# Kernel tuning notes

Measured on AMD Instinct MI355X. Metric: run time of the kernel, lower is better.

The kernel has to match this reference:

```python
import jax, jax.numpy as jnp
import numpy as np

D_MODEL = 1024
N_HEADS = 16


def setup_inputs() -> dict:
    key = jax.random.key(0)
    ks = jax.random.split(key, 5)
    B, T, C = 4, 2048, D_MODEL
    x = jax.random.normal(ks[0], (B, T, C), dtype=jnp.float32)
    s = 1.0 / np.sqrt(C)
    W_attn = jax.random.normal(ks[1], (C, 3 * C), dtype=jnp.float32) * s
    b_attn = jnp.zeros((3 * C,), dtype=jnp.float32)
    W_proj = jax.random.normal(ks[2], (C, C), dtype=jnp.float32) * s
    b_proj = jnp.zeros((C,), dtype=jnp.float32)
    return {"x": x, "W_attn": W_attn, "b_attn": b_attn, "W_proj": W_proj, "b_proj": b_proj}


def reference(x, W_attn, b_attn, W_proj, b_proj):
    B, T, C = x.shape
    H = N_HEADS
    hd = C // H
    qkv = x @ W_attn + b_attn                      # [B,T,3C]
    q, k, v = jnp.split(qkv, 3, axis=-1)
    # reshape to [B,H,T,hd]
    q = q.reshape(B, T, H, hd).transpose(0, 2, 1, 3)
    k = k.reshape(B, T, H, hd).transpose(0, 2, 1, 3)
    v = v.reshape(B, T, H, hd).transpose(0, 2, 1, 3)
    scale = 1.0 / jnp.sqrt(jnp.asarray(hd, dtype=x.dtype))
    aff = jnp.einsum('bhqd,bhkd->bhqk', q, k) * scale   # [B,H,T,T]
    causal = jnp.tril(jnp.ones((T, T), dtype=bool))
    aff = jnp.where(causal, aff, jnp.asarray(-jnp.inf, dtype=aff.dtype))
    p = jax.nn.softmax(aff, axis=-1)
    y = jnp.einsum('bhqk,bhkd->bhqd', p, v)             # [B,H,T,hd]
    y = y.transpose(0, 2, 1, 3).reshape(B, T, C)
    return y @ W_proj + b_proj
```

## Files before the change

kernel.cpp:

```cpp
#include <hip/hip_runtime.h>
#include <stdint.h>
#include <math.h>

typedef __attribute__((ext_vector_type(8))) __bf16 bf16x8;
typedef __attribute__((ext_vector_type(4))) __bf16 bf16x4;
typedef __attribute__((ext_vector_type(4))) float f32x4;
typedef __attribute__((ext_vector_type(16))) float f32x16;

#define MFMA16(A, B, C) __builtin_amdgcn_mfma_f32_16x16x32_bf16((A), (B), (C), 0, 0, 0)
#define MFMA32(A, B, C) __builtin_amdgcn_mfma_f32_32x32x16_bf16((A), (B), (C), 0, 0, 0)

#if defined(__has_builtin)
#if __has_builtin(__builtin_amdgcn_exp2f)
#define EXP2(x) __builtin_amdgcn_exp2f(x)
#else
#define EXP2(x) exp2f(x)
#endif
#else
#define EXP2(x) exp2f(x)
#endif

static constexpr int kT  = 2048;
static constexpr int kC  = 1024;
static constexpr int kHD = 64;
#define QSCALE 0.1803368801111204f

__device__ __forceinline__ void g2l16(const void* g, void* l) {
  __builtin_amdgcn_global_load_lds(
      (const __attribute__((address_space(1))) uint32_t*)g,
      (__attribute__((address_space(3))) uint32_t*)l, 16, 0, 0);
}

__global__ __launch_bounds__(256) void k_convert_x(const float* __restrict__ x,
                                                   __bf16* __restrict__ xb) {
  int i = (blockIdx.x * 256 + threadIdx.x) * 4;
  f32x4 v = *(const f32x4*)(x + i);
  bf16x4 o;
  o[0] = (__bf16)v[0]; o[1] = (__bf16)v[1]; o[2] = (__bf16)v[2]; o[3] = (__bf16)v[3];
  *(bf16x4*)(xb + i) = o;
}

__global__ __launch_bounds__(256) void k_transpose_w(const float* __restrict__ src,
                                                     __bf16* __restrict__ dst, int N) {
  __shared__ float t[32][33];
  int k0 = blockIdx.x * 32, n0 = blockIdx.y * 32;
  int c = threadIdx.x & 31, r = threadIdx.x >> 5;
#pragma unroll
  for (int i = 0; i < 4; ++i)
    t[r + i * 8][c] = src[(size_t)(k0 + r + i * 8) * N + n0 + c];
  __syncthreads();
#pragma unroll
  for (int i = 0; i < 4; ++i)
    dst[(size_t)(n0 + r + i * 8) * 1024 + k0 + c] = (__bf16)t[c][r + i * 8];
}

static constexpr int GK = 1024;
static constexpr int GNT = GK / 32;

template <int MODE>
__global__ __launch_bounds__(256, 3) void k_gemm(const __bf16* __restrict__ A,
                                                 const __bf16* __restrict__ Bw,
                                                 const float* __restrict__ bias,
                                                 __bf16* __restrict__ qo,
                                                 __bf16* __restrict__ ko,
                                                 __bf16* __restrict__ vo,
                                                 float* __restrict__ out) {
  __shared__ __bf16 As[3][128 * 32];
  __shared__ __bf16 Bs[3][128 * 32];

  const int tid = threadIdx.x;
  const int wave = tid >> 6, lane = tid & 63;
  const int lo = lane & 15, hi = lane >> 4;
  const int wr = wave & 1, wc = wave >> 1;

  constexpr int NBN = (MODE == 0) ? 24 : 8;
  const int nwg = (int)gridDim.x;
  const int id = (int)blockIdx.x;
  const int wg = (id & 7) * (nwg >> 3) + (id >> 3);
  const int bm = wg / NBN, bn = wg % NBN;
  const int m0 = bm * 128, n0 = bn * 128;

  const int rG0 = tid >> 2, gG0 = (tid & 3) ^ ((rG0 >> 1) & 3);
  const int rG1 = (tid + 256) >> 2, gG1 = ((tid + 256) & 3) ^ ((rG1 >> 1) & 3);
  const __bf16* gaA0 = A + (size_t)(m0 + rG0) * GK + gG0 * 8;
  const __bf16* gaA1 = A + (size_t)(m0 + rG1) * GK + gG1 * 8;
  const __bf16* gbB0 = Bw + (size_t)(n0 + rG0) * GK + gG0 * 8;
  const __bf16* gbB1 = Bw + (size_t)(n0 + rG1) * GK + gG1 * 8;

  const int fsw = (hi ^ ((lo >> 1) & 3)) * 8;
  const int offA = (wr * 64 + lo) * 32 + fsw;
  const int offB = (wc * 64 + lo) * 32 + fsw;

  f32x4 acc[4][4] = {};

#define GSTAGE(jt, bufi)                                  \
  {                                                       \
    g2l16(gaA0 + (jt) * 32, &As[(bufi)][tid * 8]);        \
    g2l16(gaA1 + (jt) * 32, &As[(bufi)][2048 + tid * 8]); \
    g2l16(gbB0 + (jt) * 32, &Bs[(bufi)][tid * 8]);        \
    g2l16(gbB1 + (jt) * 32, &Bs[(bufi)][2048 + tid * 8]); \
  }

  GSTAGE(0, 0);
  GSTAGE(1, 1);
  asm volatile("s_waitcnt vmcnt(4)" ::: "memory");
  __builtin_amdgcn_s_barrier();
  __builtin_amdgcn_sched_barrier(0);

  int rb = 0, rs = 2;
  for (int j = 0; j < GNT; ++j) {
    const __bf16* Ab = &As[rb][0];
    const __bf16* Bb = &Bs[rb][0];
    if (j < GNT - 2) GSTAGE(j + 2, rs);
    bf16x8 af[4], bfr[4];
#pragma unroll
    for (int m = 0; m < 4; ++m) af[m] = *(const bf16x8*)&Ab[offA + m * 512];
#pragma unroll
    for (int n = 0; n < 4; ++n) bfr[n] = *(const bf16x8*)&Bb[offB + n * 512];
    __builtin_amdgcn_s_setprio(1);
#pragma unroll
    for (int m = 0; m < 4; ++m)
#pragma unroll
      for (int n = 0; n < 4; ++n)
        acc[m][n] = MFMA16(af[m], bfr[n], acc[m][n]);
    __builtin_amdgcn_s_setprio(0);
    if (j < GNT - 2) {
      asm volatile("s_waitcnt vmcnt(4)" ::: "memory");
    } else if (j == GNT - 2) {
      asm volatile("s_waitcnt vmcnt(0)" ::: "memory");
    }
    if (j < GNT - 1) {
      __builtin_amdgcn_s_barrier();
      __builtin_amdgcn_sched_barrier(0);
    }
    rb = (rb == 2) ? 0 : rb + 1;
    rs = (rs == 2) ? 0 : rs + 1;
  }
#undef GSTAGE

  if (MODE == 0) {
#pragma unroll
    for (int nj = 0; nj < 4; ++nj) {
      int gn = n0 + wc * 64 + nj * 16 + lo;
      float bv = bias[gn];
      int which = gn >> 10;
      int c = gn & 1023;
      int hh = c >> 6, d = c & 63;
#pragma unroll
      for (int mi = 0; mi < 4; ++mi) {
        int gm = m0 + wr * 64 + mi * 16 + hi * 4;
        int bb = gm >> 11, t0 = gm & 2047;
        if (which == 2) {
          int t0p = t0 ^ ((((t0 >> 2) ^ (t0 >> 3)) & 1) * 12);
          bf16x4 vv;
#pragma unroll
          for (int r = 0; r < 4; ++r) vv[r] = (__bf16)(acc[mi][nj][r] + bv);
          *(bf16x4*)(vo + ((size_t)(bb * 16 + hh) * 64 + d) * 2048 + t0p) = vv;
        } else {
#pragma unroll
          for (int r = 0; r < 4; ++r) {
            float val = acc[mi][nj][r] + bv;
            size_t idx = (((size_t)(bb * 16 + hh)) * 2048 + (t0 + r)) * 64 + d;
            if (which == 0)
              qo[idx] = (__bf16)(val * QSCALE);
            else
              ko[idx] = (__bf16)val;
          }
        }
      }
    }
  } else {
#pragma unroll
    for (int nj = 0; nj < 4; ++nj) {
      int gn = n0 + wc * 64 + nj * 16 + lo;
      float bv = bias[gn];
#pragma unroll
      for (int mi = 0; mi < 4; ++mi) {
        int gm = m0 + wr * 64 + mi * 16 + hi * 4;
#pragma unroll
        for (int r = 0; r < 4; ++r)
          out[(size_t)(gm + r) * 1024 + gn] = acc[mi][nj][r] + bv;
      }
    }
  }
}

__global__ __launch_bounds__(256, 2) void k_flash(const __bf16* __restrict__ qb,
                                                  const __bf16* __restrict__ kb,
                                                  const __bf16* __restrict__ vt,
                                                  __bf16* __restrict__ ob) {
  __shared__ __bf16 Ks[2][64 * 64];
  __shared__ __bf16 Vs[2][64 * 64];

  const int id = (int)blockIdx.x;
  const int xcd = id & 7, jj = id >> 3;
  const int bh = (jj & 7) * 8 + xcd;
  const int xs = jj >> 3;
  const int b = bh >> 4, h = bh & 15;
  const int tid = threadIdx.x, wave = tid >> 6, lane = tid & 63;
  const int l31 = lane & 31, hi32 = lane >> 5;
  const int gx = l31 & 7;

  const int qrow[2] = { (15 - xs) * 128 + wave * 32, xs * 128 + wave * 32 };

  bf16x8 qf[2][4];
#pragma unroll
  for (int rg = 0; rg < 2; ++rg) {
    const __bf16* Qp = qb + ((size_t)bh * kT + qrow[rg] + l31) * kHD + hi32 * 8;
#pragma unroll
    for (int ks = 0; ks < 4; ++ks)
      qf[rg][ks] = *(const bf16x8*)(Qp + ks * 16);
  }

  f32x16 acc[2][2] = {};
  float srow[2] = {0.0f, 0.0f};

  const __bf16* Kbase = kb + (size_t)bh * kT * kHD;
  const __bf16* Vbase = vt + (size_t)bh * kHD * kT;

  int srcK[2], srcV[2];
#pragma unroll
  for (int p = 0; p < 2; ++p) {
    int g = wave * 64 + lane + p * 256;
    int r = g >> 3, c = g & 7;
    int cs = c ^ (r & 7);
    srcK[p] = r * kHD + cs * 8;
    srcV[p] = r * kT + cs * 8;
  }

  const int nt = 32 - 2 * xs;

#pragma unroll
  for (int p = 0; p < 2; ++p) {
    g2l16(Kbase + srcK[p], &Ks[0][wave * 512 + p * 2048]);
    g2l16(Vbase + srcV[p], &Vs[0][wave * 512 + p * 2048]);
  }

  for (int it = 0; it < nt; ++it) {
    const int kt = it * 64;
    const int pb = it & 1;
    const bool both = (it <= 2 * xs + 1);

    __syncthreads();

    if (it + 1 < nt) {
      const int kn = kt + 64;
#pragma unroll
      for (int p = 0; p < 2; ++p) {
        g2l16(Kbase + kn * kHD + srcK[p], &Ks[1 - pb][wave * 512 + p * 2048]);
        g2l16(Vbase + kn + srcV[p],       &Vs[1 - pb][wave * 512 + p * 2048]);
      }
    }

    const __bf16* Kt = &Ks[pb][0];
    const __bf16* Vt = &Vs[pb][0];

    bf16x8 pa[2][4];

#pragma unroll
    for (int kb2 = 0; kb2 < 2; ++kb2) {
      bf16x8 ka[4];
#pragma unroll
      for (int ks = 0; ks < 4; ++ks)
        ka[ks] = *(const bf16x8*)&Kt[(kb2 * 32 + l31) * 64 +
                                     (((ks * 2 + hi32) ^ gx) * 8)];
#pragma unroll
      for (int rg = 0; rg < 2; ++rg) {
        if (rg == 1 && !both) break;
        f32x16 s = {};
        __builtin_amdgcn_s_setprio(1);
#pragma unroll
        for (int ks = 0; ks < 4; ++ks) s = MFMA32(ka[ks], qf[rg][ks], s);
        __builtin_amdgcn_s_setprio(0);
        const int qg = qrow[rg] + l31;
        const int kbs = kt + kb2 * 32 + 4 * hi32;
        if (kt + kb2 * 32 + 31 > qrow[rg]) {
#pragma unroll
          for (int i = 0; i < 16; ++i)
            if (kbs + (i & 3) + 8 * (i >> 2) > qg) s[i] = -INFINITY;
        }
#pragma unroll
        for (int i = 0; i < 16; ++i) s[i] = EXP2(s[i]);
        float sm = 0.0f;
#pragma unroll
        for (int i = 0; i < 16; ++i) sm += s[i];
        srow[rg] += sm;
#pragma unroll
        for (int a = 0; a < 2; ++a) {
          bf16x8 p;
#pragma unroll
          for (int e = 0; e < 8; ++e) p[e] = (__bf16)s[8 * a + e];
          pa[rg][kb2 * 2 + a] = p;
        }
      }
    }

    __builtin_amdgcn_s_setprio(1);
#pragma unroll
    for (int db = 0; db < 2; ++db) {
#pragma unroll
      for (int ks = 0; ks < 4; ++ks) {
        bf16x8 vb = *(const bf16x8*)&Vt[(db * 32 + l31) * 64 +
                                        (((ks * 2 + hi32) ^ gx) * 8)];
        acc[0][db] = MFMA32(pa[0][ks], vb, acc[0][db]);
        if (both) acc[1][db] = MFMA32(pa[1][ks], vb, acc[1][db]);
      }
    }
    __builtin_amdgcn_s_setprio(0);
  }

#pragma unroll
  for (int rg = 0; rg < 2; ++rg) {
    float tot = srow[rg] + __shfl_xor(srow[rg], 32, 64);
    float invt = 1.0f / tot;
    __bf16* Op = ob + ((size_t)b * kT + qrow[rg]) * kC + h * kHD;
#pragma unroll
    for (int i = 0; i < 16; ++i) {
      int q = (i & 3) + 8 * (i >> 2) + 4 * hi32;
      float inv = __shfl(invt, q, 64);
      Op[(size_t)q * kC + l31]      = (__bf16)(acc[rg][0][i] * inv);
      Op[(size_t)q * kC + 32 + l31] = (__bf16)(acc[rg][1][i] * inv);
    }
  }
}

extern "C" void kernel_launch(void* const* d_in, const int* in_sizes, int n_in,
                              void* d_out, int out_size, void* d_ws, size_t ws_size,
                              hipStream_t stream) {
  const float* x      = (const float*)d_in[0];
  const float* W_attn = (const float*)d_in[1];
  const float* b_attn = (const float*)d_in[2];
  const float* W_proj = (const float*)d_in[3];
  const float* b_proj = (const float*)d_in[4];
  float* out = (float*)d_out;

  char* ws = (char*)d_ws;
  __bf16* xb  = (__bf16*)(ws + 0);
  __bf16* ob  = (__bf16*)(ws + 0);
  __bf16* wab = (__bf16*)(ws + 16777216);
  __bf16* wpb = (__bf16*)(ws + 23068672);
  __bf16* qbf = (__bf16*)(ws + 25165824);
  __bf16* kbf = (__bf16*)(ws + 41943040);
  __bf16* vtb = (__bf16*)(ws + 58720256);

  k_convert_x<<<8192, 256, 0, stream>>>(x, xb);
  k_transpose_w<<<dim3(32, 96), 256, 0, stream>>>(W_attn, wab, 3072);
  k_transpose_w<<<dim3(32, 32), 256, 0, stream>>>(W_proj, wpb, 1024);
  k_gemm<0><<<dim3(1536), 256, 0, stream>>>(xb, wab, b_attn, qbf, kbf, vtb, nullptr);
  k_flash<<<dim3(512), 256, 0, stream>>>(qbf, kbf, vtb, ob);
  k_gemm<1><<<dim3(512), 256, 0, stream>>>(ob, wpb, b_proj, nullptr, nullptr, nullptr, out);
}
```

Baseline: 241.9 us.

## Use 256x128 tiles for QKV GEMM and reorder flash block schedule

The QKV projection GEMM moves into its own kernel with a 256x128 output tile per workgroup: eight M-fragments per wave, a larger A stage buffer, and half as many workgroups, with occupancy bounds relaxed to 2. The aim is to cut global and LDS traffic per MFMA through more operand reuse, at the cost of more registers and LDS per block. Separately, the flash kernel changes the order of its xs query-split index so that blocks with different causal workloads are interleaved differently for load balance. The output projection GEMM keeps its earlier tiling as a separate kernel.

```diff
diff --git a/kernel.cpp b/kernel.cpp
--- a/kernel.cpp
+++ b/kernel.cpp
@@ -57,15 +57,13 @@
 static constexpr int GK = 1024;
 static constexpr int GNT = GK / 32;
 
-template <int MODE>
-__global__ __launch_bounds__(256, 3) void k_gemm(const __bf16* __restrict__ A,
-                                                 const __bf16* __restrict__ Bw,
-                                                 const float* __restrict__ bias,
-                                                 __bf16* __restrict__ qo,
-                                                 __bf16* __restrict__ ko,
-                                                 __bf16* __restrict__ vo,
-                                                 float* __restrict__ out) {
-  __shared__ __bf16 As[3][128 * 32];
+__global__ __launch_bounds__(256, 2) void k_gemm_qkv(const __bf16* __restrict__ A,
+                                                     const __bf16* __restrict__ Bw,
+                                                     const float* __restrict__ bias,
+                                                     __bf16* __restrict__ qo,
+                                                     __bf16* __restrict__ ko,
+                                                     __bf16* __restrict__ vo) {
+  __shared__ __bf16 As[3][256 * 32];
   __shared__ __bf16 Bs[3][128 * 32];
 
   const int tid = threadIdx.x;
@@ -73,11 +71,116 @@
   const int lo = lane & 15, hi = lane >> 4;
   const int wr = wave & 1, wc = wave >> 1;
 
-  constexpr int NBN = (MODE == 0) ? 24 : 8;
-  const int nwg = (int)gridDim.x;
   const int id = (int)blockIdx.x;
-  const int wg = (id & 7) * (nwg >> 3) + (id >> 3);
-  const int bm = wg / NBN, bn = wg % NBN;
+  const int wg = (id & 7) * 96 + (id >> 3);
+  const int bm = wg / 24, bn = wg % 24;
+  const int m0 = bm * 256, n0 = bn * 128;
+
+  const int rA = tid >> 2, cG = tid & 3;
+  const int gs = cG ^ ((rA >> 1) & 3);
+  const __bf16* ga = A + (size_t)(m0 + rA) * GK + gs * 8;
+  const __bf16* gb = Bw + (size_t)(n0 + rA) * GK + gs * 8;
+
+  const int fsw = (hi ^ ((lo >> 1) & 3)) * 8;
+  const int offA = (wr * 128 + lo) * 32 + fsw;
+  const int offB = (wc * 64 + lo) * 32 + fsw;
+
+  f32x4 acc[8][4] = {};
+
+#define QSTAGE(jt, bufi)                                                     \
+  {                                                                          \
+    g2l16(ga + (jt) * 32,                       &As[(bufi)][tid * 8]);       \
+    g2l16(ga + (jt) * 32 + (size_t)64 * GK,     &As[(bufi)][2048 + tid * 8]);\
+    g2l16(ga + (jt) * 32 + (size_t)128 * GK,    &As[(bufi)][4096 + tid * 8]);\
+    g2l16(ga + (jt) * 32 + (size_t)192 * GK,    &As[(bufi)][6144 + tid * 8]);\
+    g2l16(gb + (jt) * 32,                       &Bs[(bufi)][tid * 8]);       \
+    g2l16(gb + (jt) * 32 + (size_t)64 * GK,     &Bs[(bufi)][2048 + tid * 8]);\
+  }
+
+  QSTAGE(0, 0);
+  QSTAGE(1, 1);
+  asm volatile("s_waitcnt vmcnt(6)" ::: "memory");
+  __builtin_amdgcn_s_barrier();
+  __builtin_amdgcn_sched_barrier(0);
+
+  int rb = 0, rs = 2;
+  for (int j = 0; j < GNT; ++j) {
+    const __bf16* Ab = &As[rb][0];
+    const __bf16* Bb = &Bs[rb][0];
+    if (j < GNT - 2) QSTAGE(j + 2, rs);
+    bf16x8 af[8], bfr[4];
+#pragma unroll
+    for (int m = 0; m < 8; ++m) af[m] = *(const bf16x8*)&Ab[offA + m * 512];
+#pragma unroll
+    for (int n = 0; n < 4; ++n) bfr[n] = *(const bf16x8*)&Bb[offB + n * 512];
+    __builtin_amdgcn_s_setprio(1);
+#pragma unroll
+    for (int m = 0; m < 8; ++m)
+#pragma unroll
+      for (int n = 0; n < 4; ++n)
+        acc[m][n] = MFMA16(af[m], bfr[n], acc[m][n]);
+    __builtin_amdgcn_s_setprio(0);
+    if (j < GNT - 2) {
+      asm volatile("s_waitcnt vmcnt(6)" ::: "memory");
+    } else if (j == GNT - 2) {
+      asm volatile("s_waitcnt vmcnt(0)" ::: "memory");
+    }
+    if (j < GNT - 1) {
+      __builtin_amdgcn_s_barrier();
+      __builtin_amdgcn_sched_barrier(0);
+    }
+    rb = (rb == 2) ? 0 : rb + 1;
+    rs = (rs == 2) ? 0 : rs + 1;
+  }
+#undef QSTAGE
+
+#pragma unroll
+  for (int nj = 0; nj < 4; ++nj) {
+    int gn = n0 + wc * 64 + nj * 16 + lo;
+    float bv = bias[gn];
+    int which = gn >> 10;
+    int c = gn & 1023;
+    int hh = c >> 6, d = c & 63;
+#pragma unroll
+    for (int mi = 0; mi < 8; ++mi) {
+      int gm = m0 + wr * 128 + mi * 16 + hi * 4;
+      int bb = gm >> 11, t0 = gm & 2047;
+      if (which == 2) {
+        int t0p = t0 ^ ((((t0 >> 2) ^ (t0 >> 3)) & 1) * 12);
+        bf16x4 vv;
+#pragma unroll
+        for (int r = 0; r < 4; ++r) vv[r] = (__bf16)(acc[mi][nj][r] + bv);
+        *(bf16x4*)(vo + ((size_t)(bb * 16 + hh) * 64 + d) * 2048 + t0p) = vv;
+      } else {
+#pragma unroll
+        for (int r = 0; r < 4; ++r) {
+          float val = acc[mi][nj][r] + bv;
+          size_t idx = (((size_t)(bb * 16 + hh)) * 2048 + (t0 + r)) * 64 + d;
+          if (which == 0)
+            qo[idx] = (__bf16)(val * QSCALE);
+          else
+            ko[idx] = (__bf16)val;
+        }
+      }
+    }
+  }
+}
+
+__global__ __launch_bounds__(256, 3) void k_gemm_proj(const __bf16* __restrict__ A,
+                                                      const __bf16* __restrict__ Bw,
+                                                      const float* __restrict__ bias,
+                                                      float* __restrict__ out) {
+  __shared__ __bf16 As[3][128 * 32];
+  __shared__ __bf16 Bs[3][128 * 32];
+
+  const int tid = threadIdx.x;
+  const int wave = tid >> 6, lane = tid & 63;
+  const int lo = lane & 15, hi = lane >> 4;
+  const int wr = wave & 1, wc = wave >> 1;
+
+  const int id = (int)blockIdx.x;
+  const int wg = (id & 7) * 64 + (id >> 3);
+  const int bm = wg / 8, bn = wg % 8;
   const int m0 = bm * 128, n0 = bn * 128;
 
   const int rG0 = tid >> 2, gG0 = (tid & 3) ^ ((rG0 >> 1) & 3);
@@ -93,7 +196,7 @@
 
   f32x4 acc[4][4] = {};
 
-#define GSTAGE(jt, bufi)                                  \
+#define PSTAGE(jt, bufi)                                  \
   {                                                       \
     g2l16(gaA0 + (jt) * 32, &As[(bufi)][tid * 8]);        \
     g2l16(gaA1 + (jt) * 32, &As[(bufi)][2048 + tid * 8]); \
@@ -101,8 +204,8 @@
     g2l16(gbB1 + (jt) * 32, &Bs[(bufi)][2048 + tid * 8]); \
   }
 
-  GSTAGE(0, 0);
-  GSTAGE(1, 1);
+  PSTAGE(0, 0);
+  PSTAGE(1, 1);
   asm volatile("s_waitcnt vmcnt(4)" ::: "memory");
   __builtin_amdgcn_s_barrier();
   __builtin_amdgcn_sched_barrier(0);
@@ -111,7 +214,7 @@
   for (int j = 0; j < GNT; ++j) {
     const __bf16* Ab = &As[rb][0];
     const __bf16* Bb = &Bs[rb][0];
-    if (j < GNT - 2) GSTAGE(j + 2, rs);
+    if (j < GNT - 2) PSTAGE(j + 2, rs);
     bf16x8 af[4], bfr[4];
 #pragma unroll
     for (int m = 0; m < 4; ++m) af[m] = *(const bf16x8*)&Ab[offA + m * 512];
@@ -136,51 +239,18 @@
     rb = (rb == 2) ? 0 : rb + 1;
     rs = (rs == 2) ? 0 : rs + 1;
   }
-#undef GSTAGE
-
-  if (MODE == 0) {
-#pragma unroll
-    for (int nj = 0; nj < 4; ++nj) {
-      int gn = n0 + wc * 64 + nj * 16 + lo;
-      float bv = bias[gn];
-      int which = gn >> 10;
-      int c = gn & 1023;
-      int hh = c >> 6, d = c & 63;
-#pragma unroll
-      for (int mi = 0; mi < 4; ++mi) {
-        int gm = m0 + wr * 64 + mi * 16 + hi * 4;
-        int bb = gm >> 11, t0 = gm & 2047;
-        if (which == 2) {
-          int t0p = t0 ^ ((((t0 >> 2) ^ (t0 >> 3)) & 1) * 12);
-          bf16x4 vv;
-#pragma unroll
-          for (int r = 0; r < 4; ++r) vv[r] = (__bf16)(acc[mi][nj][r] + bv);
-          *(bf16x4*)(vo + ((size_t)(bb * 16 + hh) * 64 + d) * 2048 + t0p) = vv;
-        } else {
-#pragma unroll
-          for (int r = 0; r < 4; ++r) {
-            float val = acc[mi][nj][r] + bv;
-            size_t idx = (((size_t)(bb * 16 + hh)) * 2048 + (t0 + r)) * 64 + d;
-            if (which == 0)
-              qo[idx] = (__bf16)(val * QSCALE);
-            else
-              ko[idx] = (__bf16)val;
-          }
-        }
-      }
-    }
-  } else {
-#pragma unroll
-    for (int nj = 0; nj < 4; ++nj) {
-      int gn = n0 + wc * 64 + nj * 16 + lo;
-      float bv = bias[gn];
-#pragma unroll
-      for (int mi = 0; mi < 4; ++mi) {
-        int gm = m0 + wr * 64 + mi * 16 + hi * 4;
-#pragma unroll
-        for (int r = 0; r < 4; ++r)
-          out[(size_t)(gm + r) * 1024 + gn] = acc[mi][nj][r] + bv;
-      }
+#undef PSTAGE
+
+#pragma unroll
+  for (int nj = 0; nj < 4; ++nj) {
+    int gn = n0 + wc * 64 + nj * 16 + lo;
+    float bv = bias[gn];
+#pragma unroll
+    for (int mi = 0; mi < 4; ++mi) {
+      int gm = m0 + wr * 64 + mi * 16 + hi * 4;
+#pragma unroll
+      for (int r = 0; r < 4; ++r)
+        out[(size_t)(gm + r) * 1024 + gn] = acc[mi][nj][r] + bv;
     }
   }
 }
@@ -195,7 +265,8 @@
   const int id = (int)blockIdx.x;
   const int xcd = id & 7, jj = id >> 3;
   const int bh = (jj & 7) * 8 + xcd;
-  const int xs = jj >> 3;
+  const int xsi = jj >> 3;
+  const int xs = (xsi < 4) ? xsi : 11 - xsi;
   const int b = bh >> 4, h = bh & 15;
   const int tid = threadIdx.x, wave = tid >> 6, lane = tid & 63;
   const int l31 = lane & 31, hi32 = lane >> 5;
@@ -346,7 +417,7 @@
   k_convert_x<<<8192, 256, 0, stream>>>(x, xb);
   k_transpose_w<<<dim3(32, 96), 256, 0, stream>>>(W_attn, wab, 3072);
   k_transpose_w<<<dim3(32, 32), 256, 0, stream>>>(W_proj, wpb, 1024);
-  k_gemm<0><<<dim3(1536), 256, 0, stream>>>(xb, wab, b_attn, qbf, kbf, vtb, nullptr);
+  k_gemm_qkv<<<dim3(768), 256, 0, stream>>>(xb, wab, b_attn, qbf, kbf, vtb);
   k_flash<<<dim3(512), 256, 0, stream>>>(qbf, kbf, vtb, ob);
-  k_gemm<1><<<dim3(512), 256, 0, stream>>>(ob, wpb, b_proj, nullptr, nullptr, nullptr, out);
-}
+  k_gemm_proj<<<dim3(512), 256, 0, stream>>>(ob, wpb, b_proj, out);
+}
```

Measured after the change: 257.2 us. 6.3% more time.
